# Performance work log

Hardware: AMD Instinct MI355X
Metric: run time of the kernel (lower is better)

The kernel has to match this reference:

```python
import jax, jax.numpy as jnp
import numpy as np

B, T, D_IN = 1024, 128, 256
H = 128          # hidden_dim == memory_unit_size (required by einsum)
M = 128          # memory_units == memory_unit_size (required by view)
W = 128          # memory_unit_size
R = 4            # read_heads
OUT = 2


def setup_inputs() -> dict:
    key = jax.random.key(0)
    ks = jax.random.split(key, 9)
    s = 0.05
    return {
        "x": jax.random.normal(ks[0], (B, T, D_IN), dtype=jnp.float32),
        "memory": jax.random.normal(ks[1], (M, W), dtype=jnp.float32) * s,
        "read_vectors0": jax.random.normal(ks[2], (R, W), dtype=jnp.float32) * s,
        "W_ih": jax.random.normal(ks[3], (4 * H, D_IN + R * W), dtype=jnp.float32) * s,
        "W_hh": jax.random.normal(ks[4], (4 * H, H), dtype=jnp.float32) * s,
        "b_ih": jax.random.normal(ks[5], (4 * H,), dtype=jnp.float32) * s,
        "b_hh": jax.random.normal(ks[6], (4 * H,), dtype=jnp.float32) * s,
        "fc_w": jax.random.normal(ks[7], (OUT, H + R * W), dtype=jnp.float32) * s,
        "fc_b": jax.random.normal(ks[8], (OUT,), dtype=jnp.float32) * s,
    }


def reference(x, memory, read_vectors0, W_ih, W_hh, b_ih, b_hh, fc_w, fc_b):
    batch = x.shape[0]
    # softmax over memory slots (dim=0), constant across timesteps
    mem_sm = jax.nn.softmax(memory, axis=0)  # [M, W]
    bias = b_ih + b_hh

    # initial read vectors: [R, W] -> repeat over batch -> flatten [B, R*W]
    rv = jnp.tile(read_vectors0[None], (batch, 1, 1)).reshape(batch, R * W)
    h0 = jnp.zeros((batch, H), x.dtype)
    c0 = jnp.zeros((batch, H), x.dtype)

    def step(carry, xt):
        h, c, rv = carry
        inp = jnp.concatenate([xt, rv], axis=-1)           # [B, D_IN+R*W]
        gates = inp @ W_ih.T + h @ W_hh.T + bias           # [B, 4H]
        i, f, g, o = jnp.split(gates, 4, axis=-1)          # torch LSTM gate order
        c = jax.nn.sigmoid(f) * c + jax.nn.sigmoid(i) * jnp.tanh(g)
        h = jax.nn.sigmoid(o) * jnp.tanh(c)                # [B, H]
        read = jnp.einsum('ij,kj->ki', mem_sm, h)          # [B, M]
        # faithful to torch: repeat to [R, B, M] then view(B, R*M) (mixes rows)
        rv_new = jnp.broadcast_to(read[None], (R, batch, M)).reshape(batch, R * M)
        out = jnp.concatenate([h, rv_new], axis=-1) @ fc_w.T + fc_b  # [B, OUT]
        return (h, c, rv_new), out

    _, outs = jax.lax.scan(step, (h0, c0, rv), jnp.swapaxes(x, 0, 1))  # [T, B, OUT]
    return outs.mean(axis=0)  # [B, OUT]
```

## Files before the change

kernel.cpp:

```cpp
#include <hip/hip_runtime.h>

#define BB 1024
#define TT 128
#define NBLK 256

using bf16   = __bf16;
using bf16x8 = __attribute__((ext_vector_type(8))) bf16;
using bf16x4 = __attribute__((ext_vector_type(4))) bf16;
using f32x4  = __attribute__((ext_vector_type(4))) float;

__device__ __forceinline__ float fsig(float x) {
  return __builtin_amdgcn_rcpf(1.f + __expf(-x));
}
__device__ __forceinline__ float ftanh(float x) {
  return 2.f * __builtin_amdgcn_rcpf(1.f + __expf(-2.f * x)) - 1.f;
}

__device__ __forceinline__ void st_u32_coh(unsigned* p, unsigned v) {
  __hip_atomic_store(p, v, __ATOMIC_RELAXED, __HIP_MEMORY_SCOPE_AGENT);
}
__device__ __forceinline__ unsigned ld_u32_coh(const unsigned* p) {
  return __hip_atomic_load((unsigned*)p, __ATOMIC_RELAXED, __HIP_MEMORY_SCOPE_AGENT);
}
__device__ __forceinline__ float ld_f32_coh(const float* p) {
  return __hip_atomic_load((float*)p, __ATOMIC_RELAXED, __HIP_MEMORY_SCOPE_AGENT);
}
__device__ __forceinline__ void st_f32_coh(float* p, float v) {
  __hip_atomic_store(p, v, __ATOMIC_RELAXED, __HIP_MEMORY_SCOPE_AGENT);
}
__device__ __forceinline__ void st_u64_coh(unsigned long long* p, unsigned long long v) {
  __hip_atomic_store(p, v, __ATOMIC_RELAXED, __HIP_MEMORY_SCOPE_AGENT);
}
__device__ __forceinline__ bf16x8 ld_bf16x8_coh(const bf16* p) {
  union { unsigned long long u[2]; bf16x8 v; } c;
  c.u[0] = __hip_atomic_load((unsigned long long*)p, __ATOMIC_RELAXED, __HIP_MEMORY_SCOPE_AGENT);
  c.u[1] = __hip_atomic_load((unsigned long long*)(p + 4), __ATOMIC_RELAXED, __HIP_MEMORY_SCOPE_AGENT);
  return c.v;
}

__global__ void prep_a(const float* __restrict__ x, const float* __restrict__ mem,
                       const float* __restrict__ b_ih, const float* __restrict__ b_hh,
                       const float* __restrict__ rv0, const float* __restrict__ W_ih,
                       bf16* __restrict__ x_bf, float* __restrict__ mem_sm,
                       float* __restrict__ bias, float* __restrict__ G0,
                       unsigned* __restrict__ slots) {
  const int bid = blockIdx.x, tid = threadIdx.x;
  if (bid < 2048) {
    const int lane = tid & 63, wv = tid >> 6;
    const int wg = bid * 4 + wv;
#pragma unroll 4
    for (int r = 0; r < 16; ++r) {
      int rid = wg + r * 8192;
      int b = rid >> 7, t = rid & 127;
      int rowp = ((b >> 4) & 15) * 64 + (b >> 8) * 16 + (b & 15);
      const float4 v = *(const float4*)(x + (size_t)rid * 256 + lane * 4);
      bf16x4 o;
      o[0] = (bf16)v.x; o[1] = (bf16)v.y; o[2] = (bf16)v.z; o[3] = (bf16)v.w;
      *(bf16x4*)(x_bf + ((size_t)t * BB + rowp) * 256 + lane * 4) = o;
    }
  } else if (bid == 2048) {
    __shared__ float sM[128 * 128];
    for (int e = tid; e < 16384; e += 256) sM[e] = mem[e];
    __syncthreads();
    if (tid < 128) {
      float mx = -1e30f;
      for (int m = 0; m < 128; ++m) mx = fmaxf(mx, sM[m * 128 + tid]);
      float s = 0.f;
      for (int m = 0; m < 128; ++m) s += __expf(sM[m * 128 + tid] - mx);
      float inv = 1.f / s;
      for (int m = 0; m < 128; ++m) mem_sm[m * 128 + tid] = __expf(sM[m * 128 + tid] - mx) * inv;
    }
  } else if (bid == 2049) {
    for (int e = tid; e < 512; e += 256) bias[e] = b_ih[e] + b_hh[e];
  } else if (bid < 2052) {
    int g = (bid - 2050) * 256 + tid;
    float acc = 0.f;
    for (int k = 0; k < 512; ++k) acc += rv0[k] * W_ih[(size_t)g * 768 + 256 + k];
    G0[g] = acc;
  } else {
    for (int e = tid; e < 4096; e += 256) slots[e] = 0u;
  }
}

__global__ void prep_b(const float* __restrict__ W_ih, const float* __restrict__ fc_w,
                       const float* __restrict__ mem_sm,
                       bf16* __restrict__ WMg, float* __restrict__ FM) {
  const int bid = blockIdx.x, tid = threadIdx.x;
  if (bid < 512) {
    __shared__ float sW[512];
    const int g = bid;
    for (int e = tid; e < 512; e += 256) sW[e] = W_ih[(size_t)g * 768 + 256 + e];
    __syncthreads();
    const int r = tid >> 6, n0 = (tid & 63) * 2;
    float a0 = 0.f, a1 = 0.f;
    const float* wr = sW + r * 128;
#pragma unroll 4
    for (int m = 0; m < 128; ++m) {
      float2 ms = *(const float2*)(mem_sm + m * 128 + n0);
      a0 += wr[m] * ms.x;
      a1 += wr[m] * ms.y;
    }
    union { bf16 h[2]; unsigned u; } pk;
    pk.h[0] = (bf16)a0; pk.h[1] = (bf16)a1;
    *(unsigned*)(WMg + (size_t)g * 512 + r * 128 + n0) = pk.u;
  } else {
    for (int sub = tid; sub < 2 * 512; sub += 256) {
      int o = sub >> 9, rn = sub & 511, rr = rn >> 7, n = rn & 127;
      const float* wr = fc_w + o * 640 + 128 + rr * 128;
      float acc = 0.f;
      for (int m = 0; m < 128; ++m) acc += wr[m] * mem_sm[m * 128 + n];
      FM[o * 512 + rn] = acc;
    }
  }
}

__global__ void __launch_bounds__(256, 1) dnc_main(
    const bf16* __restrict__ x_bf, const bf16* __restrict__ WMg,
    const float* __restrict__ bias, const float* __restrict__ G0,
    const float* __restrict__ FM, bf16* __restrict__ hbuf0, bf16* __restrict__ hbuf1,
    float* __restrict__ hsumG, unsigned* __restrict__ slots,
    const float* __restrict__ W_ih, const float* __restrict__ W_hh,
    const float* __restrict__ fc_w, const float* __restrict__ fc_b,
    float* __restrict__ out) {
  __shared__ bf16 sWx[32][264];
  __shared__ bf16 sWhh[32][136];
  __shared__ bf16 sWM[32][520];
  __shared__ bf16 sHq[16][520];
  __shared__ unsigned short sStage[4][16][8];

  const int bid = blockIdx.x, tid = threadIdx.x;
  const int rt = bid >> 4, gt = bid & 15;
  const int wave = tid >> 6, lane = tid & 63;
  const int l15 = lane & 15, l4 = lane >> 4;

  auto gcol = [&](int pos) { return ((pos >> 3) << 7) + gt * 8 + (pos & 7); };

  for (int e = tid; e < 32 * 256; e += 256) sWx[e >> 8][e & 255] = (bf16)W_ih[(size_t)gcol(e >> 8) * 768 + (e & 255)];
  for (int e = tid; e < 32 * 128; e += 256) sWhh[e >> 7][e & 127] = (bf16)W_hh[gcol(e >> 7) * 128 + (e & 127)];
  for (int e = tid; e < 32 * 512; e += 256) sWM[e >> 9][e & 511] = WMg[(size_t)gcol(e >> 9) * 512 + (e & 511)];
  __syncthreads();

  const float bv0 = bias[gcol(l15)], bv1 = bias[gcol(16 + l15)];

  const bool lo = (l15 < 8);
  const int j = l15 & 7;
  const int rb = lo ? 0 : 2;
  float cst[2] = {0.f, 0.f}, hsum[2] = {0.f, 0.f};
  int growp[2];
#pragma unroll
  for (int k = 0; k < 2; ++k) growp[k] = rt * 16 + (l4 * 4 + rb + k) + 256 * wave;

  f32x4 acc0, acc1;

  auto xpart = [&](int t) {
    acc0 = f32x4{bv0, bv0, bv0, bv0};
    acc1 = f32x4{bv1, bv1, bv1, bv1};
    const bf16* xr = x_bf + ((size_t)t * BB + rt * 64 + wave * 16 + l15) * 256 + l4 * 8;
#pragma unroll
    for (int kk = 0; kk < 8; ++kk) {
      bf16x8 a  = *(const bf16x8*)(xr + kk * 32);
      bf16x8 w0 = *(const bf16x8*)&sWx[l15][kk * 32 + l4 * 8];
      bf16x8 w1 = *(const bf16x8*)&sWx[16 + l15][kk * 32 + l4 * 8];
      acc0 = __builtin_amdgcn_mfma_f32_16x16x32_bf16(a, w0, acc0, 0, 0, 0);
      acc1 = __builtin_amdgcn_mfma_f32_16x16x32_bf16(a, w1, acc1, 0, 0, 0);
    }
  };

  auto hpart = [&](const bf16* hrd) {
    bf16x8 ha[4];
    const int myrow = rt * 16 + l15 + 256 * wave;
#pragma unroll
    for (int kk = 0; kk < 4; ++kk)
      ha[kk] = ld_bf16x8_coh(hrd + ((size_t)((kk * 4 + l4) * 1024 + myrow)) * 8);
#pragma unroll
    for (int p = 0; p < 4; ++p) {
      int row64 = (lane & 15) + 16 * p;
      int seg = (lane >> 4) + 4 * wave;
      bf16x8 v = ld_bf16x8_coh(hrd + ((size_t)(seg * 1024 + rt * 64 + row64)) * 8);
      *(bf16x8*)&sHq[row64 >> 2][(row64 & 3) * 128 + seg * 8] = v;
    }
#pragma unroll
    for (int kk = 0; kk < 4; ++kk) {
      bf16x8 w0 = *(const bf16x8*)&sWhh[l15][kk * 32 + l4 * 8];
      bf16x8 w1 = *(const bf16x8*)&sWhh[16 + l15][kk * 32 + l4 * 8];
      acc0 = __builtin_amdgcn_mfma_f32_16x16x32_bf16(ha[kk], w0, acc0, 0, 0, 0);
      acc1 = __builtin_amdgcn_mfma_f32_16x16x32_bf16(ha[kk], w1, acc1, 0, 0, 0);
    }
    __syncthreads();
#pragma unroll
    for (int kk = 0; kk < 16; ++kk) {
      bf16x8 a  = *(const bf16x8*)&sHq[l15][kk * 32 + l4 * 8];
      bf16x8 w0 = *(const bf16x8*)&sWM[l15][kk * 32 + l4 * 8];
      bf16x8 w1 = *(const bf16x8*)&sWM[16 + l15][kk * 32 + l4 * 8];
      acc0 = __builtin_amdgcn_mfma_f32_16x16x32_bf16(a, w0, acc0, 0, 0, 0);
      acc1 = __builtin_amdgcn_mfma_f32_16x16x32_bf16(a, w1, acc1, 0, 0, 0);
    }
  };

  auto pw = [&](bool add_g0, bf16* hwr) {
    float o0[4], o1[4];
#pragma unroll
    for (int r = 0; r < 4; ++r) {
      o0[r] = __shfl_xor(acc0[r], 8);
      o1[r] = __shfl_xor(acc1[r], 8);
    }
    float g0i = 0.f, g0f = 0.f, g0g = 0.f, g0o = 0.f;
    if (add_g0) {
      int cb = gt * 8 + j;
      g0i = G0[cb]; g0f = G0[128 + cb]; g0g = G0[256 + cb]; g0o = G0[384 + cb];
    }
#pragma unroll
    for (int k = 0; k < 2; ++k) {
      int r = rb + k;
      float gi = (lo ? acc0[r] : o0[r]) + g0i;
      float gf = (lo ? o0[r] : acc0[r]) + g0f;
      float gg = (lo ? acc1[r] : o1[r]) + g0g;
      float go = (lo ? o1[r] : acc1[r]) + g0o;
      cst[k] = fsig(gf) * cst[k] + fsig(gi) * ftanh(gg);
      float h = fsig(go) * ftanh(cst[k]);
      hsum[k] += h;
      union { bf16 b; unsigned short u; } cv; cv.b = (bf16)h;
      sStage[wave][l4 * 4 + rb + k][j] = cv.u;
    }
    asm volatile("" ::: "memory");
    if (lane < 32) {
      unsigned long long v = *(const unsigned long long*)&sStage[wave][lane >> 1][(lane & 1) * 4];
      int row = rt * 16 + 256 * wave + (lane >> 1);
      st_u64_coh((unsigned long long*)((char*)hwr + ((size_t)(gt * 1024 + row)) * 16 + (lane & 1) * 8), v);
    }
  };

  auto commit = [&](unsigned gen) {
    asm volatile("s_waitcnt vmcnt(0)" ::: "memory");
    __syncthreads();
    if (tid == 0) st_u32_coh(slots + bid * 16, gen);
  };
  auto gridwait = [&](unsigned gen) {
    while (ld_u32_coh(slots + tid * 16) < gen) {}
    __syncthreads();
  };

  xpart(0);
  pw(true, hbuf0);
  commit(1);
  for (int t = 1; t < TT; ++t) {
    xpart(t);
    gridwait(t);
    hpart((t & 1) ? hbuf0 : hbuf1);
    pw(false, (t & 1) ? hbuf1 : hbuf0);
    commit(t + 1);
  }
#pragma unroll
  for (int k = 0; k < 2; ++k)
    st_f32_coh(hsumG + (size_t)growp[k] * 128 + gt * 8 + j, hsum[k]);
  commit(TT + 1);
  gridwait(TT + 1);
  {
    int row = bid * 4 + wave;
    const float* hsr = hsumG + (size_t)row * 128;
    const float* hqr = hsumG + (size_t)(row & 255) * 512;
    float s0 = 0.f, s1 = 0.f;
    for (int k = lane; k < 128; k += 64) { float v = ld_f32_coh(hsr + k); s0 += v * fc_w[k]; s1 += v * fc_w[640 + k]; }
    for (int k = lane; k < 512; k += 64) { float v = ld_f32_coh(hqr + k); s0 += v * FM[k]; s1 += v * FM[512 + k]; }
    for (int off = 32; off > 0; off >>= 1) { s0 += __shfl_down(s0, off); s1 += __shfl_down(s1, off); }
    if (lane == 0) {
      out[row * 2 + 0] = s0 * (1.f / 128.f) + fc_b[0];
      out[row * 2 + 1] = s1 * (1.f / 128.f) + fc_b[1];
    }
  }
}

extern "C" void kernel_launch(void* const* d_in, const int* in_sizes, int n_in,
                              void* d_out, int out_size, void* d_ws, size_t ws_size,
                              hipStream_t stream) {
  const float* x      = (const float*)d_in[0];
  const float* memory = (const float*)d_in[1];
  const float* rv0    = (const float*)d_in[2];
  const float* W_ih   = (const float*)d_in[3];
  const float* W_hh   = (const float*)d_in[4];
  const float* b_ih   = (const float*)d_in[5];
  const float* b_hh   = (const float*)d_in[6];
  const float* fc_w   = (const float*)d_in[7];
  const float* fc_b   = (const float*)d_in[8];
  float* out = (float*)d_out;
  char* ws = (char*)d_ws;

  bf16*     x_bf   = (bf16*)ws;
  bf16*     WMg    = (bf16*)(ws + 67108864);
  float*    mem_sm = (float*)(ws + 67633152);
  float*    bias   = (float*)(ws + 67698688);
  float*    G0     = (float*)(ws + 67700736);
  float*    FM     = (float*)(ws + 67702784);
  bf16*     hbuf0  = (bf16*)(ws + 67706880);
  bf16*     hbuf1  = (bf16*)(ws + 67969024);
  unsigned* slots  = (unsigned*)(ws + 68231168);
  float*    hsumG  = (float*)(ws + 68247552);

  prep_a<<<2053, 256, 0, stream>>>(x, memory, b_ih, b_hh, rv0, W_ih,
                                   x_bf, mem_sm, bias, G0, slots);
  prep_b<<<513, 256, 0, stream>>>(W_ih, fc_w, mem_sm, WMg, FM);
  dnc_main<<<NBLK, 256, 0, stream>>>(x_bf, WMg, bias, G0, FM, hbuf0, hbuf1, hsumG, slots,
                                     W_ih, W_hh, fc_w, fc_b, out);
}
```

Measured before the change: 790.8 us.

## Replace per-step grid barrier with poisoned per-timestep h buffers and dataflow polling

Drops the per-timestep grid-wide commit/gridwait barrier. Each timestep now gets its own h buffer, pre-filled with a NaN poison pattern in prep_a, and consumers spin on their own h loads until no poison lanes remain. Blocks then wait only on the data they need instead of on all 256 blocks, which removes barrier latency from the serial recurrence. The cost is a 128-slot h buffer (about 33MB) that prep_a must poison on every launch. Correctness also depends on no real bf16 h value matching the poison pattern, on the 8-byte stores being atomic, and on every block staying co-resident.

```diff
diff --git a/kernel.cpp b/kernel.cpp
--- a/kernel.cpp
+++ b/kernel.cpp
@@ -3,6 +3,7 @@
 #define BB 1024
 #define TT 128
 #define NBLK 256
+#define POISON64 0x7FC07FC07FC07FC0ULL
 
 using bf16   = __bf16;
 using bf16x8 = __attribute__((ext_vector_type(8))) bf16;
@@ -31,17 +32,19 @@
 __device__ __forceinline__ void st_u64_coh(unsigned long long* p, unsigned long long v) {
   __hip_atomic_store(p, v, __ATOMIC_RELAXED, __HIP_MEMORY_SCOPE_AGENT);
 }
-__device__ __forceinline__ bf16x8 ld_bf16x8_coh(const bf16* p) {
-  union { unsigned long long u[2]; bf16x8 v; } c;
-  c.u[0] = __hip_atomic_load((unsigned long long*)p, __ATOMIC_RELAXED, __HIP_MEMORY_SCOPE_AGENT);
-  c.u[1] = __hip_atomic_load((unsigned long long*)(p + 4), __ATOMIC_RELAXED, __HIP_MEMORY_SCOPE_AGENT);
-  return c.v;
+__device__ __forceinline__ unsigned long long ld_u64_coh(const unsigned long long* p) {
+  return __hip_atomic_load((unsigned long long*)p, __ATOMIC_RELAXED, __HIP_MEMORY_SCOPE_AGENT);
+}
+__device__ __forceinline__ bool haspoison(unsigned long long v) {
+  unsigned long long x = v ^ POISON64;
+  return ((x - 0x0001000100010001ULL) & ~x & 0x8000800080008000ULL) != 0ULL;
 }
 
 __global__ void prep_a(const float* __restrict__ x, const float* __restrict__ mem,
                        const float* __restrict__ b_ih, const float* __restrict__ b_hh,
                        const float* __restrict__ rv0, const float* __restrict__ W_ih,
-                       bf16* __restrict__ x_bf, float* __restrict__ mem_sm,
+                       bf16* __restrict__ x_bf, bf16* __restrict__ hbufs,
+                       float* __restrict__ mem_sm,
                        float* __restrict__ bias, float* __restrict__ G0,
                        unsigned* __restrict__ slots) {
   const int bid = blockIdx.x, tid = threadIdx.x;
@@ -57,6 +60,12 @@
       bf16x4 o;
       o[0] = (bf16)v.x; o[1] = (bf16)v.y; o[2] = (bf16)v.z; o[3] = (bf16)v.w;
       *(bf16x4*)(x_bf + ((size_t)t * BB + rowp) * 256 + lane * 4) = o;
+    }
+    char* pb = (char*)hbufs + (size_t)bid * 16384 + tid * 16;
+#pragma unroll
+    for (int ps = 0; ps < 4; ++ps) {
+      unsigned long long* p = (unsigned long long*)(pb + ps * 4096);
+      p[0] = POISON64; p[1] = POISON64;
     }
   } else if (bid == 2048) {
     __shared__ float sM[128 * 128];
@@ -117,7 +126,7 @@
 __global__ void __launch_bounds__(256, 1) dnc_main(
     const bf16* __restrict__ x_bf, const bf16* __restrict__ WMg,
     const float* __restrict__ bias, const float* __restrict__ G0,
-    const float* __restrict__ FM, bf16* __restrict__ hbuf0, bf16* __restrict__ hbuf1,
+    const float* __restrict__ FM, bf16* __restrict__ hbufs,
     float* __restrict__ hsumG, unsigned* __restrict__ slots,
     const float* __restrict__ W_ih, const float* __restrict__ W_hh,
     const float* __restrict__ fc_w, const float* __restrict__ fc_b,
@@ -167,24 +176,61 @@
   };
 
   auto hpart = [&](const bf16* hrd) {
-    bf16x8 ha[4];
+    const unsigned long long* hb64 = (const unsigned long long*)hrd;
     const int myrow = rt * 16 + l15 + 256 * wave;
-#pragma unroll
-    for (int kk = 0; kk < 4; ++kk)
-      ha[kk] = ld_bf16x8_coh(hrd + ((size_t)((kk * 4 + l4) * 1024 + myrow)) * 8);
+    const int seg = (lane >> 4) + 4 * wave;
+    int ia[4], ist[4];
+#pragma unroll
+    for (int kk = 0; kk < 4; ++kk) ia[kk] = ((kk * 4 + l4) * 1024 + myrow) * 2;
+#pragma unroll
+    for (int p = 0; p < 4; ++p) ist[p] = (seg * 1024 + rt * 64 + (lane & 15) + 16 * p) * 2;
+    unsigned long long va[8], vs[8];
+#pragma unroll
+    for (int kk = 0; kk < 4; ++kk) {
+      va[2 * kk]     = ld_u64_coh(hb64 + ia[kk]);
+      va[2 * kk + 1] = ld_u64_coh(hb64 + ia[kk] + 1);
+    }
+#pragma unroll
+    for (int p = 0; p < 4; ++p) {
+      vs[2 * p]     = ld_u64_coh(hb64 + ist[p]);
+      vs[2 * p + 1] = ld_u64_coh(hb64 + ist[p] + 1);
+    }
+    for (;;) {
+      unsigned st = 0;
+#pragma unroll
+      for (int i = 0; i < 8; ++i) st |= haspoison(va[i]) ? (1u << i) : 0u;
+      if (!st) break;
+      __builtin_amdgcn_s_sleep(1);
+#pragma unroll
+      for (int i = 0; i < 8; ++i)
+        if (st & (1u << i)) va[i] = ld_u64_coh(hb64 + ia[i >> 1] + (i & 1));
+    }
+#pragma unroll
+    for (int kk = 0; kk < 4; ++kk) {
+      union { unsigned long long u[2]; bf16x8 b; } c;
+      c.u[0] = va[2 * kk]; c.u[1] = va[2 * kk + 1];
+      bf16x8 w0 = *(const bf16x8*)&sWhh[l15][kk * 32 + l4 * 8];
+      bf16x8 w1 = *(const bf16x8*)&sWhh[16 + l15][kk * 32 + l4 * 8];
+      acc0 = __builtin_amdgcn_mfma_f32_16x16x32_bf16(c.b, w0, acc0, 0, 0, 0);
+      acc1 = __builtin_amdgcn_mfma_f32_16x16x32_bf16(c.b, w1, acc1, 0, 0, 0);
+    }
+    __syncthreads();
+    for (;;) {
+      unsigned st = 0;
+#pragma unroll
+      for (int i = 0; i < 8; ++i) st |= haspoison(vs[i]) ? (1u << i) : 0u;
+      if (!st) break;
+      __builtin_amdgcn_s_sleep(1);
+#pragma unroll
+      for (int i = 0; i < 8; ++i)
+        if (st & (1u << i)) vs[i] = ld_u64_coh(hb64 + ist[i >> 1] + (i & 1));
+    }
 #pragma unroll
     for (int p = 0; p < 4; ++p) {
       int row64 = (lane & 15) + 16 * p;
-      int seg = (lane >> 4) + 4 * wave;
-      bf16x8 v = ld_bf16x8_coh(hrd + ((size_t)(seg * 1024 + rt * 64 + row64)) * 8);
-      *(bf16x8*)&sHq[row64 >> 2][(row64 & 3) * 128 + seg * 8] = v;
-    }
-#pragma unroll
-    for (int kk = 0; kk < 4; ++kk) {
-      bf16x8 w0 = *(const bf16x8*)&sWhh[l15][kk * 32 + l4 * 8];
-      bf16x8 w1 = *(const bf16x8*)&sWhh[16 + l15][kk * 32 + l4 * 8];
-      acc0 = __builtin_amdgcn_mfma_f32_16x16x32_bf16(ha[kk], w0, acc0, 0, 0, 0);
-      acc1 = __builtin_amdgcn_mfma_f32_16x16x32_bf16(ha[kk], w1, acc1, 0, 0, 0);
+      union { unsigned long long u[2]; bf16x8 b; } c;
+      c.u[0] = vs[2 * p]; c.u[1] = vs[2 * p + 1];
+      *(bf16x8*)&sHq[row64 >> 2][(row64 & 3) * 128 + seg * 8] = c.b;
     }
     __syncthreads();
 #pragma unroll
@@ -230,31 +276,21 @@
     }
   };
 
-  auto commit = [&](unsigned gen) {
-    asm volatile("s_waitcnt vmcnt(0)" ::: "memory");
-    __syncthreads();
-    if (tid == 0) st_u32_coh(slots + bid * 16, gen);
-  };
-  auto gridwait = [&](unsigned gen) {
-    while (ld_u32_coh(slots + tid * 16) < gen) {}
-    __syncthreads();
-  };
-
   xpart(0);
-  pw(true, hbuf0);
-  commit(1);
+  pw(true, hbufs);
   for (int t = 1; t < TT; ++t) {
     xpart(t);
-    gridwait(t);
-    hpart((t & 1) ? hbuf0 : hbuf1);
-    pw(false, (t & 1) ? hbuf1 : hbuf0);
-    commit(t + 1);
+    hpart(hbufs + (size_t)(t - 1) * (16 * 1024 * 8));
+    pw(false, hbufs + (size_t)t * (16 * 1024 * 8));
   }
 #pragma unroll
   for (int k = 0; k < 2; ++k)
     st_f32_coh(hsumG + (size_t)growp[k] * 128 + gt * 8 + j, hsum[k]);
-  commit(TT + 1);
-  gridwait(TT + 1);
+  asm volatile("s_waitcnt vmcnt(0)" ::: "memory");
+  __syncthreads();
+  if (tid == 0) st_u32_coh(slots + bid * 16, 1u);
+  while (ld_u32_coh(slots + tid * 16) < 1u) {}
+  __syncthreads();
   {
     int row = bid * 4 + wave;
     const float* hsr = hsumG + (size_t)row * 128;
@@ -291,14 +327,13 @@
   float*    bias   = (float*)(ws + 67698688);
   float*    G0     = (float*)(ws + 67700736);
   float*    FM     = (float*)(ws + 67702784);
-  bf16*     hbuf0  = (bf16*)(ws + 67706880);
-  bf16*     hbuf1  = (bf16*)(ws + 67969024);
-  unsigned* slots  = (unsigned*)(ws + 68231168);
-  float*    hsumG  = (float*)(ws + 68247552);
+  unsigned* slots  = (unsigned*)(ws + 67706880);
+  float*    hsumG  = (float*)(ws + 67723264);
+  bf16*     hbufs  = (bf16*)(ws + 68247552);
 
   prep_a<<<2053, 256, 0, stream>>>(x, memory, b_ih, b_hh, rv0, W_ih,
-                                   x_bf, mem_sm, bias, G0, slots);
+                                   x_bf, hbufs, mem_sm, bias, G0, slots);
   prep_b<<<513, 256, 0, stream>>>(W_ih, fc_w, mem_sm, WMg, FM);
-  dnc_main<<<NBLK, 256, 0, stream>>>(x_bf, WMg, bias, G0, FM, hbuf0, hbuf1, hsumG, slots,
+  dnc_main<<<NBLK, 256, 0, stream>>>(x_bf, WMg, bias, G0, FM, hbufs, hsumG, slots,
                                      W_ih, W_hh, fc_w, fc_b, out);
 }
```

Result: faster. 747.5 us (-5.5%).
